# Performance work log

Measured on AMD Instinct MI355X. Metric: run time of the kernel, lower is better.

Reference implementation:

```python
import jax, jax.numpy as jnp
import numpy as np

H = 4096
NH = 32
HD = 128
FF = 14336
EPS = 1e-6


def _rmsnorm(x, w):
    xf = x.astype(jnp.float32)
    var = jnp.mean(xf * xf, axis=-1, keepdims=True)
    return (w * (xf * jax.lax.rsqrt(var + EPS))).astype(x.dtype)


def setup_inputs() -> dict:
    key = jax.random.key(0)
    ks = jax.random.split(key, 16)
    S = 2048
    def lin(k, fan_in, shape):
        bound = 1.0 / np.sqrt(fan_in)
        return jax.random.uniform(k, shape, jnp.float32, -bound, bound)
    return {
        "hidden_states": jax.random.normal(ks[0], (S, H), jnp.float32),
        "position_ids": jnp.arange(S, dtype=jnp.int64),
        "wq": lin(ks[1], H, (NH * HD, H)), "bq": lin(ks[2], H, (NH * HD,)),
        "wk": lin(ks[3], H, (NH * HD, H)), "bk": lin(ks[4], H, (NH * HD,)),
        "wv": lin(ks[5], H, (NH * HD, H)), "bv": lin(ks[6], H, (NH * HD,)),
        "wo": lin(ks[7], H, (H, H)), "bo": lin(ks[8], H, (H,)),
        "w_gate": lin(ks[9], H, (FF, H)),
        "w_up": lin(ks[10], H, (FF, H)),
        "w_down": lin(ks[11], FF, (H, FF)),
        "ln1_w": jnp.ones((H,), jnp.float32),
        "ln2_w": jnp.ones((H,), jnp.float32),
    }


def reference(hidden_states, position_ids, wq, bq, wk, bk, wv, bv, wo, bo,
              w_gate, w_up, w_down, ln1_w, ln2_w):
    S = hidden_states.shape[0]
    # --- attention block ---
    x = _rmsnorm(hidden_states, ln1_w)
    q = (x @ wq.T + bq).reshape(S, NH, HD)
    k = (x @ wk.T + bk).reshape(S, NH, HD)
    v = (x @ wv.T + bv).reshape(S, NH, HD)
    scale = 1.0 / np.sqrt(HD)
    scores = jnp.einsum('qhd,khd->hqk', q.astype(jnp.float32),
                        k.astype(jnp.float32)) * scale
    causal = jnp.tril(jnp.ones((S, S), bool))  # decoder causal mask
    scores = jnp.where(causal[None, :, :], scores, -jnp.inf)
    probs = jax.nn.softmax(scores, axis=-1)
    h = jnp.einsum('hqk,khd->qhd', probs, v.astype(jnp.float32))
    attn_out = h.reshape(S, NH * HD).astype(hidden_states.dtype) @ wo.T + bo
    h1 = hidden_states + attn_out
    # --- SwiGLU MLP block ---
    y = _rmsnorm(h1, ln2_w)
    mlp = (jax.nn.silu(y @ w_gate.T) * (y @ w_up.T)) @ w_down.T
    return h1 + mlp
```

## Files before the change

### kernel.cpp

```cpp
#include <hip/hip_runtime.h>
#include <math.h>

#define H_DIM 4096
#define NHEAD 32
#define HD 128
#define FF_DIM 14336

typedef unsigned short u16;
typedef __attribute__((ext_vector_type(8))) short bf16x8;
typedef __attribute__((ext_vector_type(4))) float f32x4;

typedef const __attribute__((address_space(1))) void* gas_ptr;
typedef __attribute__((address_space(3))) void* las_ptr;

__device__ __forceinline__ void gload_lds16(const void* g, void* l) {
  __builtin_amdgcn_global_load_lds((gas_ptr)g, (las_ptr)l, 16, 0, 0);
}

__device__ __forceinline__ u16 f32_to_bf16(float f) {
  unsigned int u = __float_as_uint(f);
  u = (u + 0x7FFFu + ((u >> 16) & 1u)) >> 16;
  return (u16)u;
}
__device__ __forceinline__ float bf16_to_f32(u16 x) {
  return __uint_as_float(((unsigned int)x) << 16);
}

__global__ void f2b_kernel(const float* __restrict__ in, u16* __restrict__ out, long n4) {
  long i = (long)blockIdx.x * blockDim.x + threadIdx.x;
  long stride = (long)gridDim.x * blockDim.x;
  for (; i < n4; i += stride) {
    float4 v = reinterpret_cast<const float4*>(in)[i];
    ushort4 o;
    o.x = f32_to_bf16(v.x); o.y = f32_to_bf16(v.y);
    o.z = f32_to_bf16(v.z); o.w = f32_to_bf16(v.w);
    reinterpret_cast<ushort4*>(out)[i] = o;
  }
}

__global__ void bias_concat_kernel(const float* __restrict__ a, const float* __restrict__ b,
                                   const float* __restrict__ c, float* __restrict__ out) {
  int i = blockIdx.x * blockDim.x + threadIdx.x;
  float v;
  if (i < 4096) v = a[i];
  else if (i < 8192) v = b[i - 4096];
  else v = c[i - 8192];
  out[i] = v;
}

__global__ void rmsnorm_kernel(const float* __restrict__ in, const float* __restrict__ w,
                               u16* __restrict__ out) {
  int row = blockIdx.x;
  int tid = threadIdx.x;
  const float4* x4 = reinterpret_cast<const float4*>(in + (size_t)row * H_DIM);
  float4 vv[4];
  float ss = 0.f;
#pragma unroll
  for (int it = 0; it < 4; ++it) {
    float4 v = x4[tid + it * 256];
    vv[it] = v;
    ss += v.x * v.x + v.y * v.y + v.z * v.z + v.w * v.w;
  }
#pragma unroll
  for (int off = 1; off < 64; off <<= 1) ss += __shfl_xor(ss, off);
  __shared__ float part[4];
  if ((tid & 63) == 0) part[tid >> 6] = ss;
  __syncthreads();
  float tot = part[0] + part[1] + part[2] + part[3];
  float rinv = rsqrtf(tot * (1.0f / H_DIM) + 1e-6f);
  const float4* w4 = reinterpret_cast<const float4*>(w);
  u16* orow = out + (size_t)row * H_DIM;
#pragma unroll
  for (int it = 0; it < 4; ++it) {
    float4 v = vv[it];
    float4 wv = w4[tid + it * 256];
    ushort4 o;
    o.x = f32_to_bf16(v.x * rinv * wv.x);
    o.y = f32_to_bf16(v.y * rinv * wv.y);
    o.z = f32_to_bf16(v.z * rinv * wv.z);
    o.w = f32_to_bf16(v.w * rinv * wv.w);
    reinterpret_cast<ushort4*>(orow)[tid + it * 256] = o;
  }
}

enum { EPI_QKV = 0, EPI_O = 1, EPI_SILU = 2, EPI_MUL = 3, EPI_PART = 4 };

template <int EPI, bool SPLIT>
__global__ __launch_bounds__(512, 2) void gemm256(
    const u16* __restrict__ A, const u16* __restrict__ B, void* __restrict__ outp,
    const float* __restrict__ bias, const void* __restrict__ extra,
    int M, int N, int K, int kLen) {
  __shared__ __align__(16) u16 As[2][256 * 64];
  __shared__ __align__(16) u16 Bs[2][256 * 64];
  const int tid = threadIdx.x;
  const int wid = tid >> 6, lane = tid & 63;
  const int lg = lane >> 4, li = lane & 15;
  const int wr = (wid >> 2) << 7;
  const int wc = (wid & 3) << 6;

  const int nbm = M >> 8, nbn = N >> 8;
  const int nb = nbm * nbn;
  int wg = (blockIdx.x & 7) * (gridDim.x >> 3) + (blockIdx.x >> 3);
  int s = 0;
  if (SPLIT) { s = wg / nb; wg -= s * nb; }
  const int m0 = (wg % nbm) << 8, n0 = (wg / nbm) << 8;
  const int kB = SPLIT ? s * kLen : 0;
  const int NT = kLen >> 6;

  const int r8 = tid >> 3;
  const int sl = ((tid & 7) ^ (r8 & 7)) << 3;
  const u16* sA[2][2];
  const u16* sB[2][2];
  int ldo[2][2];
#pragma unroll
  for (int P = 0; P < 2; ++P)
#pragma unroll
    for (int h = 0; h < 2; ++h) {
      int lr = P * 128 + h * 64 + r8;
      int ra = (lr & 63) | ((lr >> 1) & 64) | ((lr << 1) & 128);
      int rb = (lr & 31) | ((lr & 96) << 1) | ((lr & 128) >> 2);
      sA[P][h] = A + (size_t)(m0 + ra) * K + kB + sl;
      sB[P][h] = B + (size_t)(n0 + rb) * K + kB + sl;
      ldo[P][h] = (P * 128 + h * 64 + (wid << 3)) << 6;
    }

  auto stageA = [&](int P, int d, int ko) {
#pragma unroll
    for (int h = 0; h < 2; ++h)
      gload_lds16(sA[P][h] + ko, (void*)(&As[d][ldo[P][h]]));
  };
  auto stageB = [&](int P, int d, int ko) {
#pragma unroll
    for (int h = 0; h < 2; ++h)
      gload_lds16(sB[P][h] + ko, (void*)(&Bs[d][ldo[P][h]]));
  };

  bf16x8 a[4][2], b[4][2];
  f32x4 acc[8][4] = {};
  const int s20 = (lg ^ (li & 7)) << 3;
  const int s21 = ((4 + lg) ^ (li & 7)) << 3;

  auto ldA = [&](int d, int set) {
#pragma unroll
    for (int i = 0; i < 4; ++i) {
      int g = wr + set * 64 + i * 16;
      int lb = (g & 63) | ((g >> 1) & 64) | ((g << 1) & 128);
      const u16* base = &As[d][(lb + li) << 6];
      a[i][0] = *reinterpret_cast<const bf16x8*>(base + s20);
      a[i][1] = *reinterpret_cast<const bf16x8*>(base + s21);
    }
  };
  auto ldB = [&](int d, int set) {
#pragma unroll
    for (int jj = 0; jj < 2; ++jj) {
      int hh = wc + (set * 2 + jj) * 16;
      int lb = ((hh & 32) << 2) | ((hh & 192) >> 1) | (hh & 31);
      const u16* base = &Bs[d][(lb + li) << 6];
      b[set * 2 + jj][0] = *reinterpret_cast<const bf16x8*>(base + s20);
      b[set * 2 + jj][1] = *reinterpret_cast<const bf16x8*>(base + s21);
    }
  };
  auto mm = [&](int iset, int jset) {
    __builtin_amdgcn_s_setprio(1);
#pragma unroll
    for (int i = 0; i < 4; ++i)
#pragma unroll
      for (int jj = 0; jj < 2; ++jj)
#pragma unroll
        for (int kk = 0; kk < 2; ++kk)
          acc[iset * 4 + i][jset * 2 + jj] = __builtin_amdgcn_mfma_f32_16x16x32_bf16(
              a[i][kk], b[jset * 2 + jj][kk], acc[iset * 4 + i][jset * 2 + jj], 0, 0, 0);
    __builtin_amdgcn_s_setprio(0);
  };

  stageA(0, 0, 0); stageB(0, 0, 0); stageB(1, 0, 0); stageA(1, 0, 0);
  if (NT > 1) {
    stageA(0, 1, 64); stageB(0, 1, 64); stageB(1, 1, 64); stageA(1, 1, 64);
    asm volatile("s_waitcnt vmcnt(8)" ::: "memory");
  } else {
    asm volatile("s_waitcnt vmcnt(0)" ::: "memory");
  }
  __builtin_amdgcn_s_barrier();

  for (int t = 0; t < NT; ++t) {
    int d = t & 1;
    bool pf = (t + 2) < NT;
    int ko = (t + 2) << 6;
    ldB(d, 0); ldA(d, 0);
    __builtin_amdgcn_s_barrier();
    mm(0, 0);
    __builtin_amdgcn_s_barrier();
    ldB(d, 1);
    if (pf) { stageA(0, d, ko); stageB(0, d, ko); }
    __builtin_amdgcn_s_barrier();
    mm(0, 1);
    __builtin_amdgcn_s_barrier();
    ldA(d, 1);
    if (pf) stageB(1, d, ko);
    __builtin_amdgcn_s_barrier();
    mm(1, 0);
    __builtin_amdgcn_s_barrier();
    if (pf) {
      stageA(1, d, ko);
      asm volatile("s_waitcnt vmcnt(6)" ::: "memory");
    } else {
      asm volatile("s_waitcnt vmcnt(0)" ::: "memory");
    }
    __builtin_amdgcn_s_barrier();
    mm(1, 1);
    __builtin_amdgcn_s_barrier();
  }

#pragma unroll
  for (int i = 0; i < 8; ++i) {
#pragma unroll
    for (int j = 0; j < 4; ++j) {
      int col = n0 + wc + j * 16 + li;
      float bv = 0.f;
      if (EPI == EPI_QKV || EPI == EPI_O) bv = bias[col];
#pragma unroll
      for (int r = 0; r < 4; ++r) {
        int row = m0 + wr + i * 16 + lg * 4 + r;
        float v = acc[i][j][r] + bv;
        size_t idx = (size_t)row * N + col;
        if (EPI == EPI_QKV) {
          ((u16*)outp)[idx] = f32_to_bf16(v);
        } else if (EPI == EPI_O) {
          const float* res = (const float*)extra;
          ((float*)outp)[idx] = res[idx] + v;
        } else if (EPI == EPI_SILU) {
          float sv = v / (1.f + __expf(-v));
          ((u16*)outp)[idx] = f32_to_bf16(sv);
        } else if (EPI == EPI_MUL) {
          const u16* sg = (const u16*)extra;
          ((u16*)outp)[idx] = f32_to_bf16(v * bf16_to_f32(sg[idx]));
        } else {
          ((float*)outp)[(size_t)s * M * N + idx] = v;
        }
      }
    }
  }
}

__global__ void reduce_down(const float* __restrict__ p, const float* __restrict__ h1,
                            float* __restrict__ out, long n4, long str4) {
  long i = (long)blockIdx.x * blockDim.x + threadIdx.x;
  long st = (long)gridDim.x * blockDim.x;
  for (; i < n4; i += st) {
    float4 h = reinterpret_cast<const float4*>(h1)[i];
    float4 p0 = reinterpret_cast<const float4*>(p)[i];
    float4 p1 = reinterpret_cast<const float4*>(p)[i + str4];
    float4 o;
    o.x = h.x + p0.x + p1.x; o.y = h.y + p0.y + p1.y;
    o.z = h.z + p0.z + p1.z; o.w = h.w + p0.w + p1.w;
    reinterpret_cast<float4*>(out)[i] = o;
  }
}

__global__ void transpose_kernel(const u16* __restrict__ in, u16* __restrict__ out,
                                 int S, int ldin) {
  __shared__ __align__(16) u16 t[64][80];
  int sbT = S >> 6;
  int bs = blockIdx.x % sbT, bc = blockIdx.x / sbT;
  int s0 = bs << 6, c0 = bc << 6;
  int tid = threadIdx.x;
  int ir = tid >> 3;
  int jc = (tid & 7) * 8;
#pragma unroll
  for (int h = 0; h < 2; ++h) {
    int sr = ir + h * 32;
    uint4 v = *reinterpret_cast<const uint4*>(in + (size_t)(s0 + sr) * ldin + c0 + jc);
    *reinterpret_cast<uint4*>(&t[sr][jc]) = v;
  }
  __syncthreads();
  int d = tid >> 3;
  int ss = (tid & 7) * 8;
#pragma unroll
  for (int h = 0; h < 2; ++h) {
    int dd = d + h * 32;
    u16 tmp[8];
#pragma unroll
    for (int e = 0; e < 8; ++e) tmp[e] = t[ss + e][dd];
    *reinterpret_cast<uint4*>(out + (size_t)(c0 + dd) * S + s0 + ss) =
        *reinterpret_cast<const uint4*>(tmp);
  }
}

__global__ __launch_bounds__(256) void attn_kernel(
    const u16* __restrict__ q, const u16* __restrict__ k,
    const u16* __restrict__ vt, u16* __restrict__ o, int S, int ldqk) {
  __shared__ __align__(16) u16 plds[4][32 * 64];
  int tid = threadIdx.x, wid = tid >> 6, lane = tid & 63;
  int lg = lane >> 4, li = lane & 15;
  int nwg = gridDim.x;
  int sbid = (blockIdx.x & 7) * (nwg >> 3) + (blockIdx.x >> 3);
  int task = sbid * 4 + wid;
  int pairs = S >> 6;
  int head = task / pairs;
  int pi = task - head * pairs;
  const float scale = 0.08838834764831845f;
  u16* pl = plds[wid];

  for (int tix = 0; tix < 2; ++tix) {
    int qt = tix ? ((S >> 5) - 1 - pi) : pi;
    int q0 = qt << 5;

    bf16x8 aq[2][4];
#pragma unroll
    for (int fi = 0; fi < 2; ++fi) {
      const u16* qrow = q + (size_t)(q0 + fi * 16 + li) * ldqk + head * HD + lg * 8;
#pragma unroll
      for (int ks = 0; ks < 4; ++ks)
        aq[fi][ks] = *reinterpret_cast<const bf16x8*>(qrow + ks * 32);
    }

    f32x4 oacc[2][8] = {};
    float m_run[2][4], l_run[2][4];
#pragma unroll
    for (int fi = 0; fi < 2; ++fi)
#pragma unroll
      for (int r = 0; r < 4; ++r) { m_run[fi][r] = -INFINITY; l_run[fi][r] = 0.f; }

    int nkb = ((q0 + 31) >> 6) + 1;
    for (int kb = 0; kb < nkb; ++kb) {
      int kvbase = kb << 6;
      f32x4 sacc[2][4] = {};
#pragma unroll
      for (int cf = 0; cf < 4; ++cf) {
        const u16* krow = k + (size_t)(kvbase + cf * 16 + li) * ldqk + head * HD + lg * 8;
#pragma unroll
        for (int ks = 0; ks < 4; ++ks) {
          bf16x8 bk = *reinterpret_cast<const bf16x8*>(krow + ks * 32);
          sacc[0][cf] = __builtin_amdgcn_mfma_f32_16x16x32_bf16(aq[0][ks], bk, sacc[0][cf], 0, 0, 0);
          sacc[1][cf] = __builtin_amdgcn_mfma_f32_16x16x32_bf16(aq[1][ks], bk, sacc[1][cf], 0, 0, 0);
        }
      }
      bool bnd = (kvbase + 63) > q0;
      float alpha[2][4];
#pragma unroll
      for (int fi = 0; fi < 2; ++fi) {
#pragma unroll
        for (int r = 0; r < 4; ++r) {
          int row = q0 + fi * 16 + lg * 4 + r;
#pragma unroll
          for (int cf = 0; cf < 4; ++cf) {
            float sv = sacc[fi][cf][r] * scale;
            if (bnd && (kvbase + cf * 16 + li) > row) sv = -INFINITY;
            sacc[fi][cf][r] = sv;
          }
          float mv = fmaxf(fmaxf(sacc[fi][0][r], sacc[fi][1][r]),
                           fmaxf(sacc[fi][2][r], sacc[fi][3][r]));
#pragma unroll
          for (int off = 1; off < 16; off <<= 1) mv = fmaxf(mv, __shfl_xor(mv, off));
          float mnew = fmaxf(m_run[fi][r], mv);
          alpha[fi][r] = __expf(m_run[fi][r] - mnew);
          m_run[fi][r] = mnew;
          float ps = 0.f;
#pragma unroll
          for (int cf = 0; cf < 4; ++cf) {
            float pv = __expf(sacc[fi][cf][r] - mnew);
            sacc[fi][cf][r] = pv;
            ps += pv;
          }
#pragma unroll
          for (int off = 1; off < 16; off <<= 1) ps += __shfl_xor(ps, off);
          l_run[fi][r] = l_run[fi][r] * alpha[fi][r] + ps;
        }
      }
#pragma unroll
      for (int fi = 0; fi < 2; ++fi)
#pragma unroll
        for (int df = 0; df < 8; ++df)
#pragma unroll
          for (int r = 0; r < 4; ++r) oacc[fi][df][r] *= alpha[fi][r];
#pragma unroll
      for (int fi = 0; fi < 2; ++fi)
#pragma unroll
        for (int cf = 0; cf < 4; ++cf)
#pragma unroll
          for (int r = 0; r < 4; ++r) {
            int row = fi * 16 + lg * 4 + r;
            int el = row * 64 + cf * 16 + li;
            pl[el ^ ((row & 7) << 3)] = f32_to_bf16(sacc[fi][cf][r]);
          }
      asm volatile("s_waitcnt lgkmcnt(0)" ::: "memory");
      __builtin_amdgcn_sched_barrier(0);
#pragma unroll
      for (int kk = 0; kk < 2; ++kk) {
        bf16x8 pa[2];
#pragma unroll
        for (int fi = 0; fi < 2; ++fi) {
          int row = fi * 16 + li;
          int el = row * 64 + kk * 32 + lg * 8;
          pa[fi] = *reinterpret_cast<const bf16x8*>(pl + (el ^ ((row & 7) << 3)));
        }
        const u16* vb = vt + kvbase + kk * 32 + lg * 8;
#pragma unroll
        for (int df = 0; df < 8; ++df) {
          bf16x8 bv = *reinterpret_cast<const bf16x8*>(vb + (size_t)(head * HD + df * 16 + li) * S);
          oacc[0][df] = __builtin_amdgcn_mfma_f32_16x16x32_bf16(pa[0], bv, oacc[0][df], 0, 0, 0);
          oacc[1][df] = __builtin_amdgcn_mfma_f32_16x16x32_bf16(pa[1], bv, oacc[1][df], 0, 0, 0);
        }
      }
    }
#pragma unroll
    for (int fi = 0; fi < 2; ++fi)
#pragma unroll
      for (int r = 0; r < 4; ++r) {
        float inv = 1.0f / l_run[fi][r];
        int row = q0 + fi * 16 + lg * 4 + r;
        u16* orow = o + (size_t)row * H_DIM + head * HD;
#pragma unroll
        for (int df = 0; df < 8; ++df)
          orow[df * 16 + li] = f32_to_bf16(oacc[fi][df][r] * inv);
      }
  }
}

extern "C" void kernel_launch(void* const* d_in, const int* in_sizes, int n_in,
                              void* d_out, int out_size, void* d_ws, size_t ws_size,
                              hipStream_t stream) {
  (void)n_in; (void)out_size;
  const float* hidden = (const float*)d_in[0];
  const float* wq = (const float*)d_in[2];
  const float* bq = (const float*)d_in[3];
  const float* wk = (const float*)d_in[4];
  const float* bk = (const float*)d_in[5];
  const float* wv = (const float*)d_in[6];
  const float* bv = (const float*)d_in[7];
  const float* wo = (const float*)d_in[8];
  const float* bo = (const float*)d_in[9];
  const float* wg = (const float*)d_in[10];
  const float* wu = (const float*)d_in[11];
  const float* wd = (const float*)d_in[12];
  const float* ln1 = (const float*)d_in[13];
  const float* ln2 = (const float*)d_in[14];
  float* out = (float*)d_out;

  int S = in_sizes[0] / H_DIM;
  int NQKV = 3 * H_DIM;

  char* ws = (char*)d_ws;
  size_t off = 0;
  auto alloc = [&](size_t bytes) {
    void* p = ws + off;
    off += (bytes + 255) & ~(size_t)255;
    return p;
  };
  u16* wbuf = (u16*)alloc((size_t)FF_DIM * H_DIM * 2);
  u16* xb   = (u16*)alloc((size_t)S * H_DIM * 2);
  u16* qkv  = (u16*)alloc((size_t)S * NQKV * 2);
  u16* vtb  = (u16*)alloc((size_t)S * H_DIM * 2);
  u16* hat  = (u16*)alloc((size_t)S * H_DIM * 2);
  float* h1 = (float*)alloc((size_t)S * H_DIM * 4);
  u16* sg   = (u16*)alloc((size_t)S * FF_DIM * 2);
  u16* tb   = (u16*)alloc((size_t)S * FF_DIM * 2);
  float* bcat = (float*)alloc((size_t)NQKV * 4);
  if (off > ws_size) return;
  float* pdown = (float*)qkv;

  dim3 b256(256), b512(512);
  long nHH4 = (long)H_DIM * H_DIM / 4;
  long nFH4 = (long)FF_DIM * H_DIM / 4;
  int gQKV3 = (S / 256) * (NQKV / 256);
  int gHH   = (S / 256) * (H_DIM / 256);
  int gFF   = (S / 256) * (FF_DIM / 256);
  int gDW   = 2 * gHH;

  rmsnorm_kernel<<<S, b256, 0, stream>>>(hidden, ln1, xb);
  bias_concat_kernel<<<NQKV / 256, b256, 0, stream>>>(bq, bk, bv, bcat);
  f2b_kernel<<<4096, b256, 0, stream>>>(wq, wbuf, nHH4);
  f2b_kernel<<<4096, b256, 0, stream>>>(wk, wbuf + (size_t)H_DIM * H_DIM, nHH4);
  f2b_kernel<<<4096, b256, 0, stream>>>(wv, wbuf + (size_t)2 * H_DIM * H_DIM, nHH4);
  gemm256<EPI_QKV, false><<<gQKV3, b512, 0, stream>>>(xb, wbuf, qkv, bcat, nullptr,
                                                      S, NQKV, H_DIM, H_DIM);
  transpose_kernel<<<(S / 64) * (H_DIM / 64), b256, 0, stream>>>(qkv + 2 * H_DIM, vtb, S, NQKV);
  attn_kernel<<<(NHEAD * (S / 64)) / 4, b256, 0, stream>>>(qkv, qkv + H_DIM, vtb, hat, S, NQKV);
  f2b_kernel<<<4096, b256, 0, stream>>>(wo, wbuf, nHH4);
  gemm256<EPI_O, false><<<gHH, b512, 0, stream>>>(hat, wbuf, h1, bo, hidden,
                                                  S, H_DIM, H_DIM, H_DIM);

  rmsnorm_kernel<<<S, b256, 0, stream>>>(h1, ln2, xb);
  f2b_kernel<<<4096, b256, 0, stream>>>(wg, wbuf, nFH4);
  gemm256<EPI_SILU, false><<<gFF, b512, 0, stream>>>(xb, wbuf, sg, nullptr, nullptr,
                                                     S, FF_DIM, H_DIM, H_DIM);
  f2b_kernel<<<4096, b256, 0, stream>>>(wu, wbuf, nFH4);
  gemm256<EPI_MUL, false><<<gFF, b512, 0, stream>>>(xb, wbuf, tb, nullptr, sg,
                                                    S, FF_DIM, H_DIM, H_DIM);
  f2b_kernel<<<4096, b256, 0, stream>>>(wd, wbuf, nFH4);
  gemm256<EPI_PART, true><<<gDW, b512, 0, stream>>>(tb, wbuf, pdown, nullptr, nullptr,
                                                    S, H_DIM, FF_DIM, FF_DIM / 2);
  reduce_down<<<2048, b256, 0, stream>>>(pdown, h1, out,
                                         (long)S * H_DIM / 4, (long)S * H_DIM / 4);
}
```

Before: 1.689 ms.

## Fuse fp32-to-bf16 weight conversion into GEMM B-tile loads, split-K O-projection

Drops the separate weight conversion kernels and the bias concat. The GEMM now reads fp32 weights directly into registers, converts them to bf16 and writes them into swizzled LDS, selecting the Q/K/V weight and bias segment per block. The O projection becomes a split-K GEMM followed by a reduce that adds the residual and bias. This removes a full fp32 read plus bf16 write and re-read of every weight matrix. In exchange the B operand now travels through registers with explicit waits instead of async global-to-LDS loads, which doubles B global traffic inside the GEMM and may hurt latency hiding.

After: 2.110 ms. +24.9%, slower.

```diff
diff --git a/kernel.cpp b/kernel.cpp
--- a/kernel.cpp
+++ b/kernel.cpp
@@ -24,28 +24,6 @@
 }
 __device__ __forceinline__ float bf16_to_f32(u16 x) {
   return __uint_as_float(((unsigned int)x) << 16);
-}
-
-__global__ void f2b_kernel(const float* __restrict__ in, u16* __restrict__ out, long n4) {
-  long i = (long)blockIdx.x * blockDim.x + threadIdx.x;
-  long stride = (long)gridDim.x * blockDim.x;
-  for (; i < n4; i += stride) {
-    float4 v = reinterpret_cast<const float4*>(in)[i];
-    ushort4 o;
-    o.x = f32_to_bf16(v.x); o.y = f32_to_bf16(v.y);
-    o.z = f32_to_bf16(v.z); o.w = f32_to_bf16(v.w);
-    reinterpret_cast<ushort4*>(out)[i] = o;
-  }
-}
-
-__global__ void bias_concat_kernel(const float* __restrict__ a, const float* __restrict__ b,
-                                   const float* __restrict__ c, float* __restrict__ out) {
-  int i = blockIdx.x * blockDim.x + threadIdx.x;
-  float v;
-  if (i < 4096) v = a[i];
-  else if (i < 8192) v = b[i - 4096];
-  else v = c[i - 8192];
-  out[i] = v;
 }
 
 __global__ void rmsnorm_kernel(const float* __restrict__ in, const float* __restrict__ w,
@@ -83,13 +61,15 @@
   }
 }
 
-enum { EPI_QKV = 0, EPI_O = 1, EPI_SILU = 2, EPI_MUL = 3, EPI_PART = 4 };
+enum { EPI_QKV = 0, EPI_SILU = 2, EPI_MUL = 3, EPI_PART = 4 };
 
 template <int EPI, bool SPLIT>
 __global__ __launch_bounds__(512, 2) void gemm256(
-    const u16* __restrict__ A, const u16* __restrict__ B, void* __restrict__ outp,
-    const float* __restrict__ bias, const void* __restrict__ extra,
-    int M, int N, int K, int kLen) {
+    const u16* __restrict__ A, const float* __restrict__ Bq,
+    const float* __restrict__ Bk2, const float* __restrict__ Bv2,
+    void* __restrict__ outp, const float* __restrict__ bias_q,
+    const float* __restrict__ bias_k, const float* __restrict__ bias_v,
+    const void* __restrict__ extra, int M, int N, int K, int kLen, int NSEG) {
   __shared__ __align__(16) u16 As[2][256 * 64];
   __shared__ __align__(16) u16 Bs[2][256 * 64];
   const int tid = threadIdx.x;
@@ -98,48 +78,78 @@
   const int wr = (wid >> 2) << 7;
   const int wc = (wid & 3) << 6;
 
-  const int nbm = M >> 8, nbn = N >> 8;
-  const int nb = nbm * nbn;
+  const int nbm = M >> 8;
+  const int nb = nbm * (N >> 8);
   int wg = (blockIdx.x & 7) * (gridDim.x >> 3) + (blockIdx.x >> 3);
-  int s = 0;
-  if (SPLIT) { s = wg / nb; wg -= s * nb; }
+  int sId = 0;
+  if (SPLIT) { sId = wg / nb; wg -= sId * nb; }
   const int m0 = (wg % nbm) << 8, n0 = (wg / nbm) << 8;
-  const int kB = SPLIT ? s * kLen : 0;
+  const int kB = SPLIT ? sId * kLen : 0;
   const int NT = kLen >> 6;
 
+  const float* Bp = Bq;
+  const float* biasSel = bias_q;
+  int nn = n0;
+  if (NSEG && n0 >= NSEG) {
+    if (n0 >= 2 * NSEG) { Bp = Bv2; biasSel = bias_v; nn = n0 - 2 * NSEG; }
+    else                { Bp = Bk2; biasSel = bias_k; nn = n0 - NSEG; }
+  }
+
   const int r8 = tid >> 3;
-  const int sl = ((tid & 7) ^ (r8 & 7)) << 3;
+  const int slA = ((tid & 7) ^ (r8 & 7)) << 3;
   const u16* sA[2][2];
-  const u16* sB[2][2];
-  int ldo[2][2];
+  int ldoA[2][2];
 #pragma unroll
   for (int P = 0; P < 2; ++P)
 #pragma unroll
     for (int h = 0; h < 2; ++h) {
       int lr = P * 128 + h * 64 + r8;
       int ra = (lr & 63) | ((lr >> 1) & 64) | ((lr << 1) & 128);
-      int rb = (lr & 31) | ((lr & 96) << 1) | ((lr & 128) >> 2);
-      sA[P][h] = A + (size_t)(m0 + ra) * K + kB + sl;
-      sB[P][h] = B + (size_t)(n0 + rb) * K + kB + sl;
-      ldo[P][h] = (P * 128 + h * 64 + (wid << 3)) << 6;
-    }
-
+      sA[P][h] = A + (size_t)(m0 + ra) * K + kB + slA;
+      ldoA[P][h] = (P * 128 + h * 64 + (wid << 3)) << 6;
+    }
   auto stageA = [&](int P, int d, int ko) {
 #pragma unroll
     for (int h = 0; h < 2; ++h)
-      gload_lds16(sA[P][h] + ko, (void*)(&As[d][ldo[P][h]]));
-  };
-  auto stageB = [&](int P, int d, int ko) {
-#pragma unroll
-    for (int h = 0; h < 2; ++h)
-      gload_lds16(sB[P][h] + ko, (void*)(&Bs[d][ldo[P][h]]));
+      gload_lds16(sA[P][h] + ko, (void*)(&As[d][ldoA[P][h]]));
+  };
+
+  const int pr = tid >> 2;
+  const int q4 = tid & 3;
+  const float* srcB[2];
+#pragma unroll
+  for (int P = 0; P < 2; ++P) {
+    int lr = P * 128 + pr;
+    int rb = (lr & 31) | ((lr & 96) << 1) | ((lr & 128) >> 2);
+    srcB[P] = Bp + (size_t)(nn + rb) * K + kB + q4 * 16;
+  }
+  auto loadB = [&](int P, int ko, float4* r) {
+    const float4* s = reinterpret_cast<const float4*>(srcB[P] + ko);
+#pragma unroll
+    for (int x = 0; x < 4; ++x) r[x] = s[x];
+  };
+  auto writeB = [&](int P, int d, const float4* r) {
+    int lr = P * 128 + pr;
+    u16* base = &Bs[d][lr << 6];
+    int sw = lr & 7;
+#pragma unroll
+    for (int bb = 0; bb < 2; ++bb) {
+      u16 tmp[8];
+      const float4& u = r[bb * 2];
+      const float4& v = r[bb * 2 + 1];
+      tmp[0] = f32_to_bf16(u.x); tmp[1] = f32_to_bf16(u.y);
+      tmp[2] = f32_to_bf16(u.z); tmp[3] = f32_to_bf16(u.w);
+      tmp[4] = f32_to_bf16(v.x); tmp[5] = f32_to_bf16(v.y);
+      tmp[6] = f32_to_bf16(v.z); tmp[7] = f32_to_bf16(v.w);
+      int slot = (2 * q4 + bb) ^ sw;
+      *reinterpret_cast<bf16x8*>(base + slot * 8) = *reinterpret_cast<const bf16x8*>(tmp);
+    }
   };
 
   bf16x8 a[4][2], b[4][2];
   f32x4 acc[8][4] = {};
   const int s20 = (lg ^ (li & 7)) << 3;
   const int s21 = ((4 + lg) ^ (li & 7)) << 3;
-
   auto ldA = [&](int d, int set) {
 #pragma unroll
     for (int i = 0; i < 4; ++i) {
@@ -173,41 +183,50 @@
     __builtin_amdgcn_s_setprio(0);
   };
 
-  stageA(0, 0, 0); stageB(0, 0, 0); stageB(1, 0, 0); stageA(1, 0, 0);
-  if (NT > 1) {
-    stageA(0, 1, 64); stageB(0, 1, 64); stageB(1, 1, 64); stageA(1, 1, 64);
-    asm volatile("s_waitcnt vmcnt(8)" ::: "memory");
-  } else {
-    asm volatile("s_waitcnt vmcnt(0)" ::: "memory");
-  }
-  __builtin_amdgcn_s_barrier();
+  {
+    float4 r0[4], r1[4];
+    loadB(0, 0, r0); loadB(1, 0, r1);
+    stageA(0, 0, 0); stageA(1, 0, 0);
+    writeB(0, 0, r0); writeB(1, 0, r1);
+    if (NT > 1) {
+      loadB(0, 64, r0); loadB(1, 64, r1);
+      stageA(0, 1, 64); stageA(1, 1, 64);
+      writeB(0, 1, r0); writeB(1, 1, r1);
+    }
+    asm volatile("s_waitcnt vmcnt(0) lgkmcnt(0)" ::: "memory");
+    __builtin_amdgcn_s_barrier();
+  }
 
   for (int t = 0; t < NT; ++t) {
     int d = t & 1;
     bool pf = (t + 2) < NT;
     int ko = (t + 2) << 6;
+    float4 rb1[4], rb2[4];
     ldB(d, 0); ldA(d, 0);
+    if (pf) loadB(0, ko, rb1);
     __builtin_amdgcn_s_barrier();
     mm(0, 0);
     __builtin_amdgcn_s_barrier();
     ldB(d, 1);
-    if (pf) { stageA(0, d, ko); stageB(0, d, ko); }
+    if (pf) { stageA(0, d, ko); loadB(1, ko, rb2); }
     __builtin_amdgcn_s_barrier();
     mm(0, 1);
     __builtin_amdgcn_s_barrier();
     ldA(d, 1);
-    if (pf) stageB(1, d, ko);
+    if (pf) writeB(0, d, rb1);
     __builtin_amdgcn_s_barrier();
     mm(1, 0);
+    asm volatile("s_waitcnt lgkmcnt(0)" ::: "memory");
     __builtin_amdgcn_s_barrier();
     if (pf) {
       stageA(1, d, ko);
-      asm volatile("s_waitcnt vmcnt(6)" ::: "memory");
+      writeB(1, d, rb2);
     } else {
       asm volatile("s_waitcnt vmcnt(0)" ::: "memory");
     }
     __builtin_amdgcn_s_barrier();
     mm(1, 1);
+    asm volatile("s_waitcnt lgkmcnt(0)" ::: "memory");
     __builtin_amdgcn_s_barrier();
   }
 
@@ -216,8 +235,10 @@
 #pragma unroll
     for (int j = 0; j < 4; ++j) {
       int col = n0 + wc + j * 16 + li;
+      int bcol = nn + wc + j * 16 + li;
       float bv = 0.f;
-      if (EPI == EPI_QKV || EPI == EPI_O) bv = bias[col];
+      if (EPI == EPI_QKV) bv = biasSel[bcol];
+      if (EPI == EPI_PART && bias_q != nullptr && sId == 0) bv = biasSel[bcol];
 #pragma unroll
       for (int r = 0; r < 4; ++r) {
         int row = m0 + wr + i * 16 + lg * 4 + r;
@@ -225,9 +246,6 @@
         size_t idx = (size_t)row * N + col;
         if (EPI == EPI_QKV) {
           ((u16*)outp)[idx] = f32_to_bf16(v);
-        } else if (EPI == EPI_O) {
-          const float* res = (const float*)extra;
-          ((float*)outp)[idx] = res[idx] + v;
         } else if (EPI == EPI_SILU) {
           float sv = v / (1.f + __expf(-v));
           ((u16*)outp)[idx] = f32_to_bf16(sv);
@@ -235,19 +253,19 @@
           const u16* sg = (const u16*)extra;
           ((u16*)outp)[idx] = f32_to_bf16(v * bf16_to_f32(sg[idx]));
         } else {
-          ((float*)outp)[(size_t)s * M * N + idx] = v;
+          ((float*)outp)[(size_t)sId * M * N + idx] = v;
         }
       }
     }
   }
 }
 
-__global__ void reduce_down(const float* __restrict__ p, const float* __restrict__ h1,
+__global__ void reduce_down(const float* __restrict__ p, const float* __restrict__ res,
                             float* __restrict__ out, long n4, long str4) {
   long i = (long)blockIdx.x * blockDim.x + threadIdx.x;
   long st = (long)gridDim.x * blockDim.x;
   for (; i < n4; i += st) {
-    float4 h = reinterpret_cast<const float4*>(h1)[i];
+    float4 h = reinterpret_cast<const float4*>(res)[i];
     float4 p0 = reinterpret_cast<const float4*>(p)[i];
     float4 p1 = reinterpret_cast<const float4*>(p)[i + str4];
     float4 o;
@@ -447,49 +465,38 @@
     off += (bytes + 255) & ~(size_t)255;
     return p;
   };
-  u16* wbuf = (u16*)alloc((size_t)FF_DIM * H_DIM * 2);
-  u16* xb   = (u16*)alloc((size_t)S * H_DIM * 2);
-  u16* qkv  = (u16*)alloc((size_t)S * NQKV * 2);
-  u16* vtb  = (u16*)alloc((size_t)S * H_DIM * 2);
-  u16* hat  = (u16*)alloc((size_t)S * H_DIM * 2);
-  float* h1 = (float*)alloc((size_t)S * H_DIM * 4);
-  u16* sg   = (u16*)alloc((size_t)S * FF_DIM * 2);
-  u16* tb   = (u16*)alloc((size_t)S * FF_DIM * 2);
-  float* bcat = (float*)alloc((size_t)NQKV * 4);
+  u16* xb    = (u16*)alloc((size_t)S * H_DIM * 2);
+  u16* qkv   = (u16*)alloc((size_t)S * NQKV * 2);
+  u16* vtb   = (u16*)alloc((size_t)S * H_DIM * 2);
+  u16* hat   = (u16*)alloc((size_t)S * H_DIM * 2);
+  float* h1  = (float*)alloc((size_t)S * H_DIM * 4);
+  u16* sg    = (u16*)alloc((size_t)S * FF_DIM * 2);
+  u16* tb    = (u16*)alloc((size_t)S * FF_DIM * 2);
+  float* pbuf = (float*)alloc((size_t)2 * S * H_DIM * 4);
   if (off > ws_size) return;
-  float* pdown = (float*)qkv;
 
   dim3 b256(256), b512(512);
-  long nHH4 = (long)H_DIM * H_DIM / 4;
-  long nFH4 = (long)FF_DIM * H_DIM / 4;
   int gQKV3 = (S / 256) * (NQKV / 256);
-  int gHH   = (S / 256) * (H_DIM / 256);
+  int gO    = 2 * (S / 256) * (H_DIM / 256);
   int gFF   = (S / 256) * (FF_DIM / 256);
-  int gDW   = 2 * gHH;
+  int gDW   = 2 * (S / 256) * (H_DIM / 256);
+  long n4HH = (long)S * H_DIM / 4;
 
   rmsnorm_kernel<<<S, b256, 0, stream>>>(hidden, ln1, xb);
-  bias_concat_kernel<<<NQKV / 256, b256, 0, stream>>>(bq, bk, bv, bcat);
-  f2b_kernel<<<4096, b256, 0, stream>>>(wq, wbuf, nHH4);
-  f2b_kernel<<<4096, b256, 0, stream>>>(wk, wbuf + (size_t)H_DIM * H_DIM, nHH4);
-  f2b_kernel<<<4096, b256, 0, stream>>>(wv, wbuf + (size_t)2 * H_DIM * H_DIM, nHH4);
-  gemm256<EPI_QKV, false><<<gQKV3, b512, 0, stream>>>(xb, wbuf, qkv, bcat, nullptr,
-                                                      S, NQKV, H_DIM, H_DIM);
+  gemm256<EPI_QKV, false><<<gQKV3, b512, 0, stream>>>(
+      xb, wq, wk, wv, qkv, bq, bk, bv, nullptr, S, NQKV, H_DIM, H_DIM, H_DIM);
   transpose_kernel<<<(S / 64) * (H_DIM / 64), b256, 0, stream>>>(qkv + 2 * H_DIM, vtb, S, NQKV);
   attn_kernel<<<(NHEAD * (S / 64)) / 4, b256, 0, stream>>>(qkv, qkv + H_DIM, vtb, hat, S, NQKV);
-  f2b_kernel<<<4096, b256, 0, stream>>>(wo, wbuf, nHH4);
-  gemm256<EPI_O, false><<<gHH, b512, 0, stream>>>(hat, wbuf, h1, bo, hidden,
-                                                  S, H_DIM, H_DIM, H_DIM);
+  gemm256<EPI_PART, true><<<gO, b512, 0, stream>>>(
+      hat, wo, wo, wo, pbuf, bo, bo, bo, nullptr, S, H_DIM, H_DIM, H_DIM / 2, 0);
+  reduce_down<<<2048, b256, 0, stream>>>(pbuf, hidden, h1, n4HH, n4HH);
 
   rmsnorm_kernel<<<S, b256, 0, stream>>>(h1, ln2, xb);
-  f2b_kernel<<<4096, b256, 0, stream>>>(wg, wbuf, nFH4);
-  gemm256<EPI_SILU, false><<<gFF, b512, 0, stream>>>(xb, wbuf, sg, nullptr, nullptr,
-                                                     S, FF_DIM, H_DIM, H_DIM);
-  f2b_kernel<<<4096, b256, 0, stream>>>(wu, wbuf, nFH4);
-  gemm256<EPI_MUL, false><<<gFF, b512, 0, stream>>>(xb, wbuf, tb, nullptr, sg,
-                                                    S, FF_DIM, H_DIM, H_DIM);
-  f2b_kernel<<<4096, b256, 0, stream>>>(wd, wbuf, nFH4);
-  gemm256<EPI_PART, true><<<gDW, b512, 0, stream>>>(tb, wbuf, pdown, nullptr, nullptr,
-                                                    S, H_DIM, FF_DIM, FF_DIM / 2);
-  reduce_down<<<2048, b256, 0, stream>>>(pdown, h1, out,
-                                         (long)S * H_DIM / 4, (long)S * H_DIM / 4);
-}
+  gemm256<EPI_SILU, false><<<gFF, b512, 0, stream>>>(
+      xb, wg, wg, wg, sg, nullptr, nullptr, nullptr, nullptr, S, FF_DIM, H_DIM, H_DIM, 0);
+  gemm256<EPI_MUL, false><<<gFF, b512, 0, stream>>>(
+      xb, wu, wu, wu, tb, nullptr, nullptr, nullptr, sg, S, FF_DIM, H_DIM, H_DIM, 0);
+  gemm256<EPI_PART, true><<<gDW, b512, 0, stream>>>(
+      tb, wd, wd, wd, pbuf, nullptr, nullptr, nullptr, nullptr, S, H_DIM, FF_DIM, FF_DIM / 2, 0);
+  reduce_down<<<2048, b256, 0, stream>>>(pbuf, h1, out, n4HH, n4HH);
+}
```
